# Kernel optimization log

Measured on AMD Instinct MI355X. Metric: run time of the kernel, lower is better.

The kernel has to match this reference:

```python
import jax, jax.numpy as jnp
import numpy as np

B, H, M, K = 256, 1024, 20, 20  # batch, hidden, max_ingr, pairing top_k (must be equal: M==K)
VOCAB, INGR_V = 32000, 5000


def setup_inputs() -> dict:
    key = jax.random.key(0)
    ks = jax.random.split(key, 24)
    s = 0.02
    inp = {
        "input_ids": jax.random.randint(ks[0], (1, B), 0, VOCAB),
        "hidden": jax.random.normal(ks[1], (1, B, H), jnp.float32),
        "encoder_outputs": jax.random.normal(ks[2], (M, B, 2 * H), jnp.float32),
        "input_tensor": jax.random.randint(ks[3], (B, M), 0, INGR_V),
        "pairing_ids": jax.random.randint(ks[4], (INGR_V, K), 0, INGR_V),
        # parameters
        "emb_dec": jax.random.normal(ks[5], (VOCAB, H), jnp.float32) * s,
        "enc_emb": jax.random.normal(ks[6], (INGR_V, 2 * H), jnp.float32) * s,
        "Wq_i": jax.random.normal(ks[7], (H, H), jnp.float32) * s,
        "Wk_i": jax.random.normal(ks[8], (2 * H, H), jnp.float32) * s,
        "wa_i": jax.random.normal(ks[9], (H,), jnp.float32) * s,
        "Wq_p": jax.random.normal(ks[10], (H, H), jnp.float32) * s,
        "Wk_p": jax.random.normal(ks[11], (2 * H, H), jnp.float32) * s,
        "wa_p": jax.random.normal(ks[12], (H,), jnp.float32) * s,
        "ba_p": jax.random.normal(ks[13], (), jnp.float32) * s,
        "W_lin": jax.random.normal(ks[14], (3 * H, 2 * H), jnp.float32) * s,
        "b_lin": jnp.zeros((2 * H,), jnp.float32),
        "W_ih": jax.random.normal(ks[15], (3 * H, 2 * H), jnp.float32) * s,
        "W_hh": jax.random.normal(ks[16], (3 * H, H), jnp.float32) * s,
        "b_ih": jnp.zeros((3 * H,), jnp.float32),
        "b_hh": jnp.zeros((3 * H,), jnp.float32),
        "W_out": jax.random.normal(ks[17], (H, VOCAB), jnp.float32) * s,
        "b_out": jnp.zeros((VOCAB,), jnp.float32),
    }
    return inp


def reference(input_ids, hidden, encoder_outputs, input_tensor, pairing_ids,
              emb_dec, enc_emb, Wq_i, Wk_i, wa_i, Wq_p, Wk_p, wa_p, ba_p,
              W_lin, b_lin, W_ih, W_hh, b_ih, b_hh, W_out, b_out):
    h = hidden[0]                              # (B, H)
    emb = jnp.take(emb_dec, input_ids[0], axis=0)  # (B, H)

    # ---- IngrAtt (additive attention over ingredients) ----
    # torch code does a raw .view(B, M, 2H) on a (M, B, 2H) tensor -> plain reshape
    enc = encoder_outputs.reshape(B, M, 2 * H)
    query = h @ Wq_i                           # (B, H)
    key = enc @ Wk_i                           # (B, M, H)
    scores_i = jnp.tanh(query[:, None, :] + key) @ wa_i  # (B, M)
    aw = jax.nn.softmax(scores_i, axis=-1)     # (B, M)

    # ---- retrieval: pick most-attended ingredient, gather its top-k pairings ----
    ingr_arg = jnp.argmax(aw, axis=1)                          # (B,)
    ingr_id = input_tensor[jnp.arange(B), ingr_arg]            # (B,)
    comp_ids = jnp.take(pairing_ids, ingr_id, axis=0)          # (B, K)
    comp_emb = jnp.take(enc_emb, comp_ids, axis=0)             # (B, K, 2H)

    # ---- PairingAtt ----
    q_p = h @ Wq_p                             # (B, H)
    k_p = comp_emb @ Wk_p                      # (B, K, H)
    s_p = jnp.tanh(q_p[:, None, :] + k_p) @ wa_p + ba_p  # (B, K)
    a_p = jax.nn.softmax(s_p, axis=-1)
    attn_scores = a_p * s_p                    # (B, K) softmax-weighted raw scores
    attn_app = jnp.einsum('bk,bkd->bd', attn_scores, comp_emb)  # (B, 2H)

    out_pair = jnp.concatenate([emb, attn_app], axis=-1)  # (B, 3H)
    x = out_pair @ W_lin + b_lin                           # (B, 2H) -> GRU input

    # ---- single GRU step (torch gate ordering r,z,n) ----
    gi = x @ W_ih.T + b_ih
    gh = h @ W_hh.T + b_hh
    i_r, i_z, i_n = jnp.split(gi, 3, axis=-1)
    h_r, h_z, h_n = jnp.split(gh, 3, axis=-1)
    r = jax.nn.sigmoid(i_r + h_r)
    z = jax.nn.sigmoid(i_z + h_z)
    n = jnp.tanh(i_n + r * h_n)
    h_new = (1.0 - z) * n + z * h              # (B, H)

    logits = h_new @ W_out + b_out             # (B, VOCAB)
    return logits
```

## Files before the change

kernel.cpp:

```cpp
#include <hip/hip_runtime.h>
#include <cstdio>


using f32x4   = __attribute__((ext_vector_type(4))) float;
using bf16x8  = __attribute__((ext_vector_type(8))) short;
using ushort8 = __attribute__((ext_vector_type(8))) unsigned short;

__device__ __forceinline__ unsigned short f2bf(float x) {
    unsigned u = __builtin_bit_cast(unsigned, x);
    u += 0x7fffu + ((u >> 16) & 1u);
    return (unsigned short)(u >> 16);
}
__device__ __forceinline__ float bf2f(unsigned short u) {
    return __builtin_bit_cast(float, ((unsigned)u) << 16);
}

__device__ __forceinline__ void gload16(const void* g, void* l) {
    auto gp = (const __attribute__((address_space(1))) void*)g;
    auto lp = (__attribute__((address_space(3))) void*)l;
    __builtin_amdgcn_global_load_lds(gp, lp, 16, 0, 0);
}

__global__ __launch_bounds__(256) void prep_conv_kernel(
    const float* __restrict__ hidden, const float* __restrict__ enc_out,
    const float* __restrict__ enc_emb,
    unsigned short* __restrict__ hb, unsigned short* __restrict__ encb,
    unsigned short* __restrict__ encembb)
{
    int i = blockIdx.x * 256 + threadIdx.x;
    const float* src; unsigned short* dst; int j;
    if (i < 65536)            { src = hidden;  dst = hb;      j = i; }
    else if (i < 2686976)     { src = enc_out; dst = encb;    j = i - 65536; }
    else                      { src = enc_emb; dst = encembb; j = i - 2686976; }
    float4 v = ((const float4*)src)[j];
    ((ushort4*)dst)[j] = make_ushort4(f2bf(v.x), f2bf(v.y), f2bf(v.z), f2bf(v.w));
}

__global__ __launch_bounds__(256) void conv2w_kernel(
    const float* __restrict__ Wih, const float* __restrict__ Whh,
    unsigned short* __restrict__ ob0, unsigned short* __restrict__ ob1)
{
    int i = blockIdx.x * 256 + threadIdx.x;
    const float* src; unsigned short* dst; int j;
    if (i < 1572864) { src = Wih; dst = ob0; j = i; }
    else             { src = Whh; dst = ob1; j = i - 1572864; }
    float4 v = ((const float4*)src)[j];
    ((ushort4*)dst)[j] = make_ushort4(f2bf(v.x), f2bf(v.y), f2bf(v.z), f2bf(v.w));
}

__device__ __forceinline__ void transpose_body(
    const float* __restrict__ in, unsigned short* __restrict__ out, int R, int C)
{
    __shared__ float t[32][129];
    const int tid = threadIdx.x;
    const int c0 = blockIdx.x * 32, r0 = blockIdx.y * 128;
    const int lr = tid >> 3;
    const int cc = (tid & 7) * 4;
    #pragma unroll
    for (int i = 0; i < 4; ++i) {
        int r = lr + 32 * i;
        float4 v = *(const float4*)(in + (size_t)(r0 + r) * C + c0 + cc);
        t[cc + 0][r] = v.x; t[cc + 1][r] = v.y;
        t[cc + 2][r] = v.z; t[cc + 3][r] = v.w;
    }
    __syncthreads();
    const int rc = (tid & 15) * 8;
    #pragma unroll
    for (int p = 0; p < 2; ++p) {
        int c = (tid >> 4) + 16 * p;
        const float* src = &t[c][rc];
        ushort8 o;
        #pragma unroll
        for (int j = 0; j < 8; ++j) o[j] = f2bf(src[j]);
        *(ushort8*)(out + (size_t)(c0 + c) * R + r0 + rc) = o;
    }
}
__global__ __launch_bounds__(256) void transpose1_kernel(
    const float* in, unsigned short* out, int R, int C)
{ transpose_body(in, out, R, C); }

__global__ __launch_bounds__(256) void transpose2_kernel(
    const float* in0, const float* in1, unsigned short* out0, unsigned short* out1,
    int R, int C)
{ transpose_body(blockIdx.z ? in1 : in0, blockIdx.z ? out1 : out0, R, C); }

template<int OUTBF, bool HAS_BIAS>
__device__ __forceinline__ void gemm_core(
    const unsigned short* __restrict__ A, const unsigned short* __restrict__ Bt,
    const float* __restrict__ bias, void* __restrict__ Cout, int Ncols,
    int sA, int sB, int kLen,
    unsigned short* lA0, unsigned short* lA1,
    unsigned short* lB0, unsigned short* lB1)
{
    const int tid = threadIdx.x;
    const int lane = tid & 63, wave = tid >> 6;
    const int wr = wave >> 1, wc = wave & 1;
    const int m0 = blockIdx.y * 128, n0 = blockIdx.x * 128;
    const int srow = tid >> 3, schunk = tid & 7;
    const int lm = lane & 15, lk = (lane >> 4) * 8;

    f32x4 acc[4][4];
    #pragma unroll
    for (int m = 0; m < 4; ++m)
        #pragma unroll
        for (int n = 0; n < 4; ++n) { f32x4 z = {0.f,0.f,0.f,0.f}; acc[m][n] = z; }

    const unsigned short* Ag = A  + (size_t)(m0 + srow) * sA + schunk * 8;
    const unsigned short* Bg = Bt + (size_t)(n0 + srow) * sB + schunk * 8;
    const int nt = kLen >> 6;

    auto stage = [&](unsigned short* la_, unsigned short* lb_, int t) {
        char* la = (char*)la_ + tid * 16;
        char* lb = (char*)lb_ + tid * 16;
        #pragma unroll
        for (int i = 0; i < 4; ++i) {
            gload16(Ag + (size_t)(32 * i) * sA + t * 64, la + i * 4096);
            gload16(Bg + (size_t)(32 * i) * sB + t * 64, lb + i * 4096);
        }
    };
    auto compute = [&](const unsigned short* la_, const unsigned short* lb_) {
        #pragma unroll
        for (int kk = 0; kk < 2; ++kk) {
            bf16x8 af[4], bv[4];
            #pragma unroll
            for (int m = 0; m < 4; ++m)
                af[m] = *(const bf16x8*)((const char*)la_ +
                          (wr * 64 + m * 16 + lm) * 128 + (kk * 32 + lk) * 2);
            #pragma unroll
            for (int n = 0; n < 4; ++n)
                bv[n] = *(const bf16x8*)((const char*)lb_ +
                          (wc * 64 + n * 16 + lm) * 128 + (kk * 32 + lk) * 2);
            #pragma unroll
            for (int m = 0; m < 4; ++m)
                #pragma unroll
                for (int n = 0; n < 4; ++n)
                    acc[m][n] = __builtin_amdgcn_mfma_f32_16x16x32_bf16(
                        af[m], bv[n], acc[m][n], 0, 0, 0);
        }
    };

    stage(lA0, lB0, 0);
    __syncthreads();
    for (int t = 0; t < nt; t += 2) {
        if (t + 1 < nt) stage(lA1, lB1, t + 1);
        compute(lA0, lB0);
        __syncthreads();
        if (t + 1 < nt) {
            if (t + 2 < nt) stage(lA0, lB0, t + 2);
            compute(lA1, lB1);
            __syncthreads();
        }
    }

    const int rbase = m0 + wr * 64 + (lane >> 4) * 4;
    const int cbase = n0 + wc * 64 + lm;
    #pragma unroll
    for (int m = 0; m < 4; ++m) {
        #pragma unroll
        for (int n = 0; n < 4; ++n) {
            int col = cbase + n * 16;
            float bvv = HAS_BIAS ? bias[col] : 0.0f;
            #pragma unroll
            for (int j = 0; j < 4; ++j) {
                int row = rbase + m * 16 + j;
                float v = acc[m][n][j] + bvv;
                if (OUTBF)
                    ((unsigned short*)Cout)[(size_t)row * Ncols + col] = f2bf(v);
                else
                    ((float*)Cout)[(size_t)row * Ncols + col] = v;
            }
        }
    }
}

#define GEMM_SHARED \
    __shared__ unsigned short lA0[8192]; __shared__ unsigned short lA1[8192]; \
    __shared__ unsigned short lB0[8192]; __shared__ unsigned short lB1[8192];

__global__ __launch_bounds__(256) void gemm_dual_kernel(
    const unsigned short* A, const unsigned short* B0, const unsigned short* B1,
    float* P0, float* P1)
{
    GEMM_SHARED
    const int g = blockIdx.z >> 2, s = blockIdx.z & 3;
    const unsigned short* Bt = (g ? B1 : B0) + s * 256;
    float* C = (g ? P1 : P0) + (size_t)s * 262144;
    gemm_core<0,false>(A + s * 256, Bt, nullptr, C, 1024, 1024, 1024, 256,
                       lA0, lA1, lB0, lB1);
}

__global__ __launch_bounds__(256) void reduceq_kernel(
    const float* __restrict__ pqQ, const float* __restrict__ pqP,
    float* __restrict__ query, float* __restrict__ qp)
{
    int i = blockIdx.x * 256 + threadIdx.x;
    const float4* p; float4* o; int j;
    if (i < 65536) { p = (const float4*)pqQ; o = (float4*)query; j = i; }
    else           { p = (const float4*)pqP; o = (float4*)qp;    j = i - 65536; }
    float4 a = p[j], b = p[j + 65536], c = p[j + 131072], d = p[j + 196608];
    o[j] = make_float4(a.x + b.x + c.x + d.x, a.y + b.y + c.y + d.y,
                       a.z + b.z + c.z + d.z, a.w + b.w + c.w + d.w);
}

__global__ __launch_bounds__(256) void gemm24_kernel(
    const unsigned short* encembb, const unsigned short* encb,
    const unsigned short* WkpT, const unsigned short* WkiT,
    unsigned short* kp_all, unsigned short* key)
{
    GEMM_SHARED
    const int z = blockIdx.z;
    const unsigned short* A  = z ? encb : encembb;
    const unsigned short* Bt = z ? WkiT : WkpT;
    unsigned short* C = z ? key : kp_all;
    gemm_core<1,false>(A, Bt, nullptr, C, 1024, 2048, 2048, 2048,
                       lA0, lA1, lB0, lB1);
}

__global__ __launch_bounds__(256) void gemm5_kernel(
    const unsigned short* A, const unsigned short* Bt, float* P)
{
    GEMM_SHARED
    const int z = blockIdx.z;
    gemm_core<0,false>(A + z * 768, Bt + z * 768, nullptr,
                       P + (size_t)z * 524288, 2048, 3072, 3072, 768,
                       lA0, lA1, lB0, lB1);
}

__global__ __launch_bounds__(256) void gemm67_kernel(
    const unsigned short* xb, const unsigned short* hb,
    const unsigned short* Wih, const unsigned short* Whh, float* pg)
{
    GEMM_SHARED
    const int g = blockIdx.z >> 1, s = blockIdx.z & 1;
    const unsigned short* A  = g ? hb  + s * 512 : xb  + s * 1024;
    const unsigned short* Bt = g ? Whh + s * 512 : Wih + s * 1024;
    const int sAB  = g ? 1024 : 2048;
    const int kLen = g ? 512  : 1024;
    float* C = pg + (size_t)blockIdx.z * 786432;
    gemm_core<0,false>(A, Bt, nullptr, C, 3072, sAB, sAB, kLen, lA0, lA1, lB0, lB1);
}

__global__ __launch_bounds__(512) void gemm8_fused_kernel(
    const unsigned short* __restrict__ A, const float* __restrict__ Wout,
    const float* __restrict__ bias, float* __restrict__ C)
{
    __shared__ unsigned short lA0[16384]; __shared__ unsigned short lA1[16384];
    __shared__ unsigned short lB0[8192];  __shared__ unsigned short lB1[8192];
    const int tid  = threadIdx.x;
    const int lane = tid & 63, wave = tid >> 6;
    const int wr = wave >> 1, wc = wave & 1;
    const int n0 = blockIdx.x * 128;
    const int lm = lane & 15, lk = (lane >> 4) * 8;
    const int srow = tid >> 3, schunk = tid & 7;
    const int bcol = tid & 127, bko = tid >> 7;
    const int bsw  = (bcol & 7) << 4;

    f32x4 acc[4][4];
    #pragma unroll
    for (int m = 0; m < 4; ++m)
        #pragma unroll
        for (int n = 0; n < 4; ++n) { f32x4 z = {0.f,0.f,0.f,0.f}; acc[m][n] = z; }

    const unsigned short* Ag = A + (size_t)srow * 1024 + schunk * 8;

    auto stageA = [&](unsigned short* la_, int t) {
        char* la = (char*)la_ + tid * 16;
        #pragma unroll
        for (int i = 0; i < 4; ++i)
            gload16(Ag + (size_t)(64 * i) * 1024 + t * 64, la + i * 8192);
    };
    float bv_[16];
    auto loadB = [&](int t) {
        const float* src = Wout + (size_t)(t * 64 + bko * 16) * 32000 + n0 + bcol;
        #pragma unroll
        for (int j = 0; j < 16; ++j) bv_[j] = src[(size_t)j * 32000];
    };
    auto writeB = [&](unsigned short* lb_) {
        ushort8 o0, o1;
        #pragma unroll
        for (int j = 0; j < 8; ++j) { o0[j] = f2bf(bv_[j]); o1[j] = f2bf(bv_[j + 8]); }
        char* base = (char*)lb_ + bcol * 128;
        *(ushort8*)(base + ((bko * 32)      ^ bsw)) = o0;
        *(ushort8*)(base + ((bko * 32 + 16) ^ bsw)) = o1;
    };
    auto compute = [&](const unsigned short* la_, const unsigned short* lb_) {
        #pragma unroll
        for (int kk = 0; kk < 2; ++kk) {
            bf16x8 af[4], bv[4];
            #pragma unroll
            for (int m = 0; m < 4; ++m)
                af[m] = *(const bf16x8*)((const char*)la_ +
                          (wr * 64 + m * 16 + lm) * 128 + (kk * 32 + lk) * 2);
            #pragma unroll
            for (int n = 0; n < 4; ++n) {
                int r = wc * 64 + n * 16 + lm;
                bv[n] = *(const bf16x8*)((const char*)lb_ +
                          r * 128 + (((kk * 32 + lk) * 2) ^ ((r & 7) << 4)));
            }
            #pragma unroll
            for (int m = 0; m < 4; ++m)
                #pragma unroll
                for (int n = 0; n < 4; ++n)
                    acc[m][n] = __builtin_amdgcn_mfma_f32_16x16x32_bf16(
                        af[m], bv[n], acc[m][n], 0, 0, 0);
        }
    };

    stageA(lA0, 0); loadB(0); writeB(lB0);
    __syncthreads();
    const int nt = 16;
    for (int t = 0; t < nt; t += 2) {
        if (t + 1 < nt) { stageA(lA1, t + 1); loadB(t + 1); }
        compute(lA0, lB0);
        if (t + 1 < nt) writeB(lB1);
        __syncthreads();
        if (t + 1 < nt) {
            if (t + 2 < nt) { stageA(lA0, t + 2); loadB(t + 2); }
            compute(lA1, lB1);
            if (t + 2 < nt) writeB(lB0);
            __syncthreads();
        }
    }

    const int rbase = wr * 64 + (lane >> 4) * 4;
    const int cbase = n0 + wc * 64 + lm;
    #pragma unroll
    for (int m = 0; m < 4; ++m) {
        #pragma unroll
        for (int n = 0; n < 4; ++n) {
            int col = cbase + n * 16;
            float bvv = bias[col];
            #pragma unroll
            for (int j = 0; j < 4; ++j)
                C[(size_t)(rbase + m * 16 + j) * 32000 + col] = acc[m][n][j] + bvv;
        }
    }
}

__global__ __launch_bounds__(256) void attn_scores_kernel(
    const float* __restrict__ q, const unsigned short* __restrict__ k,
    const float* __restrict__ wa, float* __restrict__ scores)
{
    const int bm = blockIdx.x;
    const int b  = bm / 20;
    const int tid = threadIdx.x;
    float4 qv  = ((const float4*)(q + (size_t)b * 1024))[tid];
    ushort4 kv = ((const ushort4*)(k + (size_t)bm * 1024))[tid];
    float4 wv  = ((const float4*)wa)[tid];
    float p = tanhf(qv.x + bf2f(kv.x)) * wv.x + tanhf(qv.y + bf2f(kv.y)) * wv.y
            + tanhf(qv.z + bf2f(kv.z)) * wv.z + tanhf(qv.w + bf2f(kv.w)) * wv.w;
    #pragma unroll
    for (int off = 32; off > 0; off >>= 1) p += __shfl_down(p, off);
    __shared__ float sp[4];
    if ((tid & 63) == 0) sp[tid >> 6] = p;
    __syncthreads();
    if (tid == 0) scores[bm] = sp[0] + sp[1] + sp[2] + sp[3];
}

__device__ __forceinline__ int argmax_ing(
    const float* __restrict__ sc_i, const int* __restrict__ input_tensor, int b)
{
    float best = sc_i[b * 20]; int bi = 0;
    #pragma unroll
    for (int m = 1; m < 20; ++m) {
        float v = sc_i[b * 20 + m];
        if (v > best) { best = v; bi = m; }
    }
    return input_tensor[b * 20 + bi];
}

__global__ __launch_bounds__(256) void attn_scores_gather_kernel(
    const float* __restrict__ q, const unsigned short* __restrict__ kp_all,
    const float* __restrict__ wa, const float* __restrict__ ba,
    const float* __restrict__ sc_i, const int* __restrict__ input_tensor,
    const int* __restrict__ pairing_ids, float* __restrict__ scores)
{
    const int bm = blockIdx.x;
    const int b  = bm / 20;
    const int kk = bm - b * 20;
    const int tid = threadIdx.x;
    const int ing = argmax_ing(sc_i, input_tensor, b);
    const int cid = pairing_ids[ing * 20 + kk];
    float4 qv  = ((const float4*)(q + (size_t)b * 1024))[tid];
    ushort4 kv = ((const ushort4*)(kp_all + (size_t)cid * 1024))[tid];
    float4 wv  = ((const float4*)wa)[tid];
    float p = tanhf(qv.x + bf2f(kv.x)) * wv.x + tanhf(qv.y + bf2f(kv.y)) * wv.y
            + tanhf(qv.z + bf2f(kv.z)) * wv.z + tanhf(qv.w + bf2f(kv.w)) * wv.w;
    #pragma unroll
    for (int off = 32; off > 0; off >>= 1) p += __shfl_down(p, off);
    __shared__ float sp[4];
    if ((tid & 63) == 0) sp[tid >> 6] = p;
    __syncthreads();
    if (tid == 0) scores[bm] = sp[0] + sp[1] + sp[2] + sp[3] + ba[0];
}

__global__ __launch_bounds__(256) void out_pair_kernel(
    const float* __restrict__ s_p, const float* __restrict__ enc_emb,
    const float* __restrict__ sc_i, const int* __restrict__ input_tensor,
    const int* __restrict__ pairing_ids,
    const float* __restrict__ emb_dec, const int* __restrict__ input_ids,
    unsigned short* __restrict__ out_pairb)
{
    const int b = blockIdx.x / 6, seg = blockIdx.x % 6;
    const int tid = threadIdx.x;
    const int d = seg * 512 + tid * 2;
    ushort2 o;
    if (seg < 2) {
        float2 v = *(const float2*)(emb_dec + (size_t)input_ids[b] * 1024 + d);
        o.x = f2bf(v.x); o.y = f2bf(v.y);
    } else {
        const int ing = argmax_ing(sc_i, input_tensor, b);
        __shared__ float s_raw[20];
        if (tid < 20) s_raw[tid] = s_p[b * 20 + tid];
        __syncthreads();
        float mx = -1e30f;
        #pragma unroll
        for (int m = 0; m < 20; ++m) mx = fmaxf(mx, s_raw[m]);
        float den = 0.f; float w[20];
        #pragma unroll
        for (int m = 0; m < 20; ++m) { w[m] = expf(s_raw[m] - mx); den += w[m]; }
        const float inv = 1.f / den;
        const int dd = d - 1024;
        float a0 = 0.f, a1 = 0.f;
        #pragma unroll
        for (int k = 0; k < 20; ++k) {
            const int cid = pairing_ids[ing * 20 + k];
            float2 v = *(const float2*)(enc_emb + (size_t)cid * 2048 + dd);
            float a = w[k] * inv * s_raw[k];
            a0 += a * v.x; a1 += a * v.y;
        }
        o.x = f2bf(a0); o.y = f2bf(a1);
    }
    *(ushort2*)(out_pairb + (size_t)b * 3072 + d) = o;
}

__global__ __launch_bounds__(256) void reduce5_kernel(
    const float* __restrict__ P, const float* __restrict__ bias,
    unsigned short* __restrict__ xb)
{
    int i = blockIdx.x * 256 + threadIdx.x;
    const float4* p = (const float4*)P;
    float4 a = p[i], b = p[i + 131072], c = p[i + 262144], d = p[i + 393216];
    float4 bb = ((const float4*)bias)[i & 511];
    ((ushort4*)xb)[i] = make_ushort4(f2bf(a.x + b.x + c.x + d.x + bb.x),
                                     f2bf(a.y + b.y + c.y + d.y + bb.y),
                                     f2bf(a.z + b.z + c.z + d.z + bb.z),
                                     f2bf(a.w + b.w + c.w + d.w + bb.w));
}

__global__ __launch_bounds__(256) void gru_kernel(
    const float* __restrict__ pg, const float* __restrict__ b_ih,
    const float* __restrict__ b_hh, const float* __restrict__ h,
    unsigned short* __restrict__ hnewb)
{
    int idx = blockIdx.x * 256 + threadIdx.x;
    int b = idx >> 10, j = idx & 1023;
    const float* gi0 = pg + (size_t)b * 3072;
    const float* gi1 = gi0 + 786432;
    const float* gh0 = gi0 + 2 * 786432;
    const float* gh1 = gi0 + 3 * 786432;
    float ir  = gi0[j]        + gi1[j]        + b_ih[j];
    float iz  = gi0[1024 + j] + gi1[1024 + j] + b_ih[1024 + j];
    float in_ = gi0[2048 + j] + gi1[2048 + j] + b_ih[2048 + j];
    float hr  = gh0[j]        + gh1[j]        + b_hh[j];
    float hz  = gh0[1024 + j] + gh1[1024 + j] + b_hh[1024 + j];
    float hn  = gh0[2048 + j] + gh1[2048 + j] + b_hh[2048 + j];
    float r = 1.f / (1.f + expf(-(ir + hr)));
    float z = 1.f / (1.f + expf(-(iz + hz)));
    float n = tanhf(in_ + r * hn);
    hnewb[idx] = f2bf((1.f - z) * n + z * h[idx]);
}

extern "C" void kernel_launch(void* const* d_in, const int* in_sizes, int n_in,
                              void* d_out, int out_size, void* d_ws, size_t ws_size,
                              hipStream_t stream)
{
    const int*   input_ids    = (const int*)  d_in[0];
    const float* hidden       = (const float*)d_in[1];
    const float* enc_out      = (const float*)d_in[2];
    const int*   input_tensor = (const int*)  d_in[3];
    const int*   pairing_ids  = (const int*)  d_in[4];
    const float* emb_dec      = (const float*)d_in[5];
    const float* enc_emb      = (const float*)d_in[6];
    const float* Wq_i  = (const float*)d_in[7];
    const float* Wk_i  = (const float*)d_in[8];
    const float* wa_i  = (const float*)d_in[9];
    const float* Wq_p  = (const float*)d_in[10];
    const float* Wk_p  = (const float*)d_in[11];
    const float* wa_p  = (const float*)d_in[12];
    const float* ba_p  = (const float*)d_in[13];
    const float* W_lin = (const float*)d_in[14];
    const float* b_lin = (const float*)d_in[15];
    const float* W_ih  = (const float*)d_in[16];
    const float* W_hh  = (const float*)d_in[17];
    const float* b_ih  = (const float*)d_in[18];
    const float* b_hh  = (const float*)d_in[19];
    const float* W_out = (const float*)d_in[20];
    const float* b_out = (const float*)d_in[21];

    constexpr size_t OFF_HB    = 0;
    constexpr size_t OFF_HNEW  = 524288;
    constexpr size_t OFF_WQI   = 1048576;
    constexpr size_t OFF_WQP   = 3145728;
    constexpr size_t OFF_WKI   = 5242880;
    constexpr size_t OFF_WKP   = 9437184;
    constexpr size_t OFF_ENC   = 13631488;
    constexpr size_t OFF_SLOT1 = 34603008;
    constexpr size_t OFF_SLOT2 = 55574528;
    constexpr size_t OFF_QUERY = 76546048;
    constexpr size_t OFF_QP    = 77594624;
    constexpr size_t OFF_SCI   = 78643200;
    constexpr size_t OFF_SCP   = 78667776;
    constexpr size_t OFF_PGI   = 1048576;
    constexpr size_t NEED      = 79167488;
    if (ws_size < NEED) {
        fprintf(stderr, "kernel_launch: ws_size %zu < needed %zu\n", ws_size, NEED);
        return;
    }
    char* ws = (char*)d_ws;
    unsigned short* hb     = (unsigned short*)(ws + OFF_HB);
    unsigned short* hnewb  = (unsigned short*)(ws + OFF_HNEW);
    unsigned short* WqiT   = (unsigned short*)(ws + OFF_WQI);
    unsigned short* WqpT   = (unsigned short*)(ws + OFF_WQP);
    float*          pqQ    = (float*)         (ws + OFF_WKI);
    float*          pqP    = (float*)         (ws + OFF_WKP);
    unsigned short* WkiT   = (unsigned short*)(ws + OFF_WKI);
    unsigned short* WkpT   = (unsigned short*)(ws + OFF_WKP);
    unsigned short* encb   = (unsigned short*)(ws + OFF_ENC);
    unsigned short* kp_all = (unsigned short*)(ws + OFF_SLOT1);
    unsigned short* key    = (unsigned short*)(ws + OFF_SLOT1 + 10485760);
    unsigned short* encembb= (unsigned short*)(ws + OFF_SLOT2);
    unsigned short* WlinT  = (unsigned short*)(ws + OFF_SLOT2);
    unsigned short* Wihb   = (unsigned short*)(ws + OFF_SLOT2);
    unsigned short* Whhb   = (unsigned short*)(ws + OFF_SLOT2 + 12582912);
    unsigned short* outp   = (unsigned short*)(ws + OFF_SLOT1);
    float*          pG5    = (float*)         (ws + OFF_SLOT1 + 1572864);
    unsigned short* xb     = (unsigned short*)(ws + OFF_SLOT1 + 9961472);
    float*          query  = (float*)         (ws + OFF_QUERY);
    float*          qp     = (float*)         (ws + OFF_QP);
    float*          sc_i   = (float*)         (ws + OFF_SCI);
    float*          sc_p   = (float*)         (ws + OFF_SCP);
    float*          pgi    = (float*)         (ws + OFF_PGI);

    prep_conv_kernel<<<20496, 256, 0, stream>>>(hidden, enc_out, enc_emb,
                                                hb, encb, encembb);

    transpose2_kernel<<<dim3(32, 8, 2), 256, 0, stream>>>(Wq_i, Wq_p, WqiT, WqpT, 1024, 1024);
    gemm_dual_kernel<<<dim3(8, 2, 8), 256, 0, stream>>>(hb, WqiT, WqpT, pqQ, pqP);
    reduceq_kernel<<<512, 256, 0, stream>>>(pqQ, pqP, query, qp);

    transpose2_kernel<<<dim3(32, 16, 2), 256, 0, stream>>>(Wk_i, Wk_p, WkiT, WkpT, 2048, 1024);

    gemm24_kernel<<<dim3(8, 40, 2), 256, 0, stream>>>(encembb, encb, WkpT, WkiT,
                                                      kp_all, key);

    attn_scores_kernel<<<5120, 256, 0, stream>>>(query, key, wa_i, sc_i);
    attn_scores_gather_kernel<<<5120, 256, 0, stream>>>(qp, kp_all, wa_p, ba_p,
                                                        sc_i, input_tensor, pairing_ids, sc_p);

    out_pair_kernel<<<1536, 256, 0, stream>>>(sc_p, enc_emb, sc_i, input_tensor,
                                              pairing_ids, emb_dec, input_ids, outp);

    transpose1_kernel<<<dim3(64, 24), 256, 0, stream>>>(W_lin, WlinT, 3072, 2048);
    gemm5_kernel<<<dim3(16, 2, 4), 256, 0, stream>>>(outp, WlinT, pG5);
    reduce5_kernel<<<512, 256, 0, stream>>>(pG5, b_lin, xb);

    conv2w_kernel<<<9216, 256, 0, stream>>>(W_ih, W_hh, Wihb, Whhb);
    gemm67_kernel<<<dim3(24, 2, 4), 256, 0, stream>>>(xb, hb, Wihb, Whhb, pgi);

    gru_kernel<<<1024, 256, 0, stream>>>(pgi, b_ih, b_hh, hidden, hnewb);

    gemm8_fused_kernel<<<250, 512, 0, stream>>>(hnewb, W_out, b_out, (float*)d_out);
}
```

Measured before the change: 257.5 us.

## Fuse prep transposes, remap gemm24 blocks per XCD, deepen split-K, retile output GEMM

Merges the activation bf16 conversion and the Wq/Wk transposes into one prep launch, which saves two launches. The gemm24 grid is flattened and remapped so each XCD works on a contiguous band of M tiles, aiming for better L2 reuse. Split-K depth is doubled for gemm5 and gemm67, with the reduce and GRU kernels summing more partials, so small GEMMs fill more CUs at the cost of extra partial-sum traffic. The final vocab GEMM moves from 512-thread 128-column tiles to 256-thread 64-column tiles with 500 blocks, which raises occupancy but re-reads the hidden-state A tile more often.

```diff
diff --git a/kernel.cpp b/kernel.cpp
--- a/kernel.cpp
+++ b/kernel.cpp
@@ -21,20 +21,69 @@
     __builtin_amdgcn_global_load_lds(gp, lp, 16, 0, 0);
 }
 
-__global__ __launch_bounds__(256) void prep_conv_kernel(
+__device__ __forceinline__ void transpose_body(
+    const float* __restrict__ in, unsigned short* __restrict__ out,
+    int R, int C, int r0, int c0)
+{
+    __shared__ float t[32][129];
+    const int tid = threadIdx.x;
+    const int lr = tid >> 3;
+    const int cc = (tid & 7) * 4;
+    #pragma unroll
+    for (int i = 0; i < 4; ++i) {
+        int r = lr + 32 * i;
+        float4 v = *(const float4*)(in + (size_t)(r0 + r) * C + c0 + cc);
+        t[cc + 0][r] = v.x; t[cc + 1][r] = v.y;
+        t[cc + 2][r] = v.z; t[cc + 3][r] = v.w;
+    }
+    __syncthreads();
+    const int rc = (tid & 15) * 8;
+    #pragma unroll
+    for (int p = 0; p < 2; ++p) {
+        int c = (tid >> 4) + 16 * p;
+        const float* src = &t[c][rc];
+        ushort8 o;
+        #pragma unroll
+        for (int j = 0; j < 8; ++j) o[j] = f2bf(src[j]);
+        *(ushort8*)(out + (size_t)(c0 + c) * R + r0 + rc) = o;
+    }
+}
+
+__global__ __launch_bounds__(256) void prep1_kernel(
     const float* __restrict__ hidden, const float* __restrict__ enc_out,
     const float* __restrict__ enc_emb,
+    const float* __restrict__ Wq_i, const float* __restrict__ Wq_p,
+    const float* __restrict__ Wk_i, const float* __restrict__ Wk_p,
     unsigned short* __restrict__ hb, unsigned short* __restrict__ encb,
-    unsigned short* __restrict__ encembb)
-{
-    int i = blockIdx.x * 256 + threadIdx.x;
-    const float* src; unsigned short* dst; int j;
-    if (i < 65536)            { src = hidden;  dst = hb;      j = i; }
-    else if (i < 2686976)     { src = enc_out; dst = encb;    j = i - 65536; }
-    else                      { src = enc_emb; dst = encembb; j = i - 2686976; }
-    float4 v = ((const float4*)src)[j];
-    ((ushort4*)dst)[j] = make_ushort4(f2bf(v.x), f2bf(v.y), f2bf(v.z), f2bf(v.w));
-}
+    unsigned short* __restrict__ encembb,
+    unsigned short* __restrict__ WqiT, unsigned short* __restrict__ WqpT,
+    unsigned short* __restrict__ WkiT, unsigned short* __restrict__ WkpT)
+{
+    const int bid = blockIdx.x;
+    if (bid < 20496) {
+        int i = bid * 256 + threadIdx.x;
+        const float* src; unsigned short* dst; int j;
+        if (i < 65536)        { src = hidden;  dst = hb;      j = i; }
+        else if (i < 2686976) { src = enc_out; dst = encb;    j = i - 65536; }
+        else                  { src = enc_emb; dst = encembb; j = i - 2686976; }
+        float4 v = ((const float4*)src)[j];
+        ((ushort4*)dst)[j] = make_ushort4(f2bf(v.x), f2bf(v.y), f2bf(v.z), f2bf(v.w));
+    } else if (bid < 21008) {
+        int local = bid - 20496;
+        int bz = local >> 8, rem = local & 255;
+        transpose_body(bz ? Wq_p : Wq_i, bz ? WqpT : WqiT,
+                       1024, 1024, (rem >> 5) * 128, (rem & 31) * 32);
+    } else {
+        int local = bid - 21008;
+        int bz = local >> 9, rem = local & 511;
+        transpose_body(bz ? Wk_p : Wk_i, bz ? WkpT : WkiT,
+                       2048, 1024, (rem >> 5) * 128, (rem & 31) * 32);
+    }
+}
+
+__global__ __launch_bounds__(256) void transpose1_kernel(
+    const float* in, unsigned short* out, int R, int C)
+{ transpose_body(in, out, R, C, blockIdx.y * 128, blockIdx.x * 32); }
 
 __global__ __launch_bounds__(256) void conv2w_kernel(
     const float* __restrict__ Wih, const float* __restrict__ Whh,
@@ -48,54 +97,17 @@
     ((ushort4*)dst)[j] = make_ushort4(f2bf(v.x), f2bf(v.y), f2bf(v.z), f2bf(v.w));
 }
 
-__device__ __forceinline__ void transpose_body(
-    const float* __restrict__ in, unsigned short* __restrict__ out, int R, int C)
-{
-    __shared__ float t[32][129];
-    const int tid = threadIdx.x;
-    const int c0 = blockIdx.x * 32, r0 = blockIdx.y * 128;
-    const int lr = tid >> 3;
-    const int cc = (tid & 7) * 4;
-    #pragma unroll
-    for (int i = 0; i < 4; ++i) {
-        int r = lr + 32 * i;
-        float4 v = *(const float4*)(in + (size_t)(r0 + r) * C + c0 + cc);
-        t[cc + 0][r] = v.x; t[cc + 1][r] = v.y;
-        t[cc + 2][r] = v.z; t[cc + 3][r] = v.w;
-    }
-    __syncthreads();
-    const int rc = (tid & 15) * 8;
-    #pragma unroll
-    for (int p = 0; p < 2; ++p) {
-        int c = (tid >> 4) + 16 * p;
-        const float* src = &t[c][rc];
-        ushort8 o;
-        #pragma unroll
-        for (int j = 0; j < 8; ++j) o[j] = f2bf(src[j]);
-        *(ushort8*)(out + (size_t)(c0 + c) * R + r0 + rc) = o;
-    }
-}
-__global__ __launch_bounds__(256) void transpose1_kernel(
-    const float* in, unsigned short* out, int R, int C)
-{ transpose_body(in, out, R, C); }
-
-__global__ __launch_bounds__(256) void transpose2_kernel(
-    const float* in0, const float* in1, unsigned short* out0, unsigned short* out1,
-    int R, int C)
-{ transpose_body(blockIdx.z ? in1 : in0, blockIdx.z ? out1 : out0, R, C); }
-
 template<int OUTBF, bool HAS_BIAS>
 __device__ __forceinline__ void gemm_core(
     const unsigned short* __restrict__ A, const unsigned short* __restrict__ Bt,
     const float* __restrict__ bias, void* __restrict__ Cout, int Ncols,
-    int sA, int sB, int kLen,
+    int sA, int sB, int kLen, int m0, int n0,
     unsigned short* lA0, unsigned short* lA1,
     unsigned short* lB0, unsigned short* lB1)
 {
     const int tid = threadIdx.x;
     const int lane = tid & 63, wave = tid >> 6;
     const int wr = wave >> 1, wc = wave & 1;
-    const int m0 = blockIdx.y * 128, n0 = blockIdx.x * 128;
     const int srow = tid >> 3, schunk = tid & 7;
     const int lm = lane & 15, lk = (lane >> 4) * 8;
 
@@ -186,7 +198,7 @@
     const unsigned short* Bt = (g ? B1 : B0) + s * 256;
     float* C = (g ? P1 : P0) + (size_t)s * 262144;
     gemm_core<0,false>(A + s * 256, Bt, nullptr, C, 1024, 1024, 1024, 256,
-                       lA0, lA1, lB0, lB1);
+                       blockIdx.y * 128, blockIdx.x * 128, lA0, lA1, lB0, lB1);
 }
 
 __global__ __launch_bounds__(256) void reduceq_kernel(
@@ -208,12 +220,17 @@
     unsigned short* kp_all, unsigned short* key)
 {
     GEMM_SHARED
-    const int z = blockIdx.z;
+    const int id  = blockIdx.x;
+    const int xcd = id & 7;
+    const int z   = xcd >> 2, q = xcd & 3;
+    const int r   = id >> 3;
+    const int mi  = q * 10 + (r >> 3);
+    const int n   = r & 7;
     const unsigned short* A  = z ? encb : encembb;
     const unsigned short* Bt = z ? WkiT : WkpT;
     unsigned short* C = z ? key : kp_all;
     gemm_core<1,false>(A, Bt, nullptr, C, 1024, 2048, 2048, 2048,
-                       lA0, lA1, lB0, lB1);
+                       mi * 128, n * 128, lA0, lA1, lB0, lB1);
 }
 
 __global__ __launch_bounds__(256) void gemm5_kernel(
@@ -221,9 +238,9 @@
 {
     GEMM_SHARED
     const int z = blockIdx.z;
-    gemm_core<0,false>(A + z * 768, Bt + z * 768, nullptr,
-                       P + (size_t)z * 524288, 2048, 3072, 3072, 768,
-                       lA0, lA1, lB0, lB1);
+    gemm_core<0,false>(A + z * 384, Bt + z * 384, nullptr,
+                       P + (size_t)z * 524288, 2048, 3072, 3072, 384,
+                       blockIdx.y * 128, blockIdx.x * 128, lA0, lA1, lB0, lB1);
 }
 
 __global__ __launch_bounds__(256) void gemm67_kernel(
@@ -231,28 +248,28 @@
     const unsigned short* Wih, const unsigned short* Whh, float* pg)
 {
     GEMM_SHARED
-    const int g = blockIdx.z >> 1, s = blockIdx.z & 1;
-    const unsigned short* A  = g ? hb  + s * 512 : xb  + s * 1024;
-    const unsigned short* Bt = g ? Whh + s * 512 : Wih + s * 1024;
+    const int g = blockIdx.z >> 2, s = blockIdx.z & 3;
+    const unsigned short* A  = g ? hb  + s * 256 : xb  + s * 512;
+    const unsigned short* Bt = g ? Whh + s * 256 : Wih + s * 512;
     const int sAB  = g ? 1024 : 2048;
-    const int kLen = g ? 512  : 1024;
+    const int kLen = g ? 256  : 512;
     float* C = pg + (size_t)blockIdx.z * 786432;
-    gemm_core<0,false>(A, Bt, nullptr, C, 3072, sAB, sAB, kLen, lA0, lA1, lB0, lB1);
-}
-
-__global__ __launch_bounds__(512) void gemm8_fused_kernel(
+    gemm_core<0,false>(A, Bt, nullptr, C, 3072, sAB, sAB, kLen,
+                       blockIdx.y * 128, blockIdx.x * 128, lA0, lA1, lB0, lB1);
+}
+
+__global__ __launch_bounds__(256) void gemm8_kernel(
     const unsigned short* __restrict__ A, const float* __restrict__ Wout,
     const float* __restrict__ bias, float* __restrict__ C)
 {
     __shared__ unsigned short lA0[16384]; __shared__ unsigned short lA1[16384];
-    __shared__ unsigned short lB0[8192];  __shared__ unsigned short lB1[8192];
+    __shared__ unsigned short lB0[4096];  __shared__ unsigned short lB1[4096];
     const int tid  = threadIdx.x;
     const int lane = tid & 63, wave = tid >> 6;
-    const int wr = wave >> 1, wc = wave & 1;
-    const int n0 = blockIdx.x * 128;
+    const int n0 = blockIdx.x * 64;
     const int lm = lane & 15, lk = (lane >> 4) * 8;
     const int srow = tid >> 3, schunk = tid & 7;
-    const int bcol = tid & 127, bko = tid >> 7;
+    const int bcol = tid & 63, bkg = tid >> 6;
     const int bsw  = (bcol & 7) << 4;
 
     f32x4 acc[4][4];
@@ -266,12 +283,12 @@
     auto stageA = [&](unsigned short* la_, int t) {
         char* la = (char*)la_ + tid * 16;
         #pragma unroll
-        for (int i = 0; i < 4; ++i)
-            gload16(Ag + (size_t)(64 * i) * 1024 + t * 64, la + i * 8192);
+        for (int i = 0; i < 8; ++i)
+            gload16(Ag + (size_t)(32 * i) * 1024 + t * 64, la + i * 4096);
     };
     float bv_[16];
     auto loadB = [&](int t) {
-        const float* src = Wout + (size_t)(t * 64 + bko * 16) * 32000 + n0 + bcol;
+        const float* src = Wout + (size_t)(t * 64 + bkg * 16) * 32000 + n0 + bcol;
         #pragma unroll
         for (int j = 0; j < 16; ++j) bv_[j] = src[(size_t)j * 32000];
     };
@@ -280,8 +297,8 @@
         #pragma unroll
         for (int j = 0; j < 8; ++j) { o0[j] = f2bf(bv_[j]); o1[j] = f2bf(bv_[j + 8]); }
         char* base = (char*)lb_ + bcol * 128;
-        *(ushort8*)(base + ((bko * 32)      ^ bsw)) = o0;
-        *(ushort8*)(base + ((bko * 32 + 16) ^ bsw)) = o1;
+        *(ushort8*)(base + ((bkg * 32)      ^ bsw)) = o0;
+        *(ushort8*)(base + ((bkg * 32 + 16) ^ bsw)) = o1;
     };
     auto compute = [&](const unsigned short* la_, const unsigned short* lb_) {
         #pragma unroll
@@ -290,12 +307,12 @@
             #pragma unroll
             for (int m = 0; m < 4; ++m)
                 af[m] = *(const bf16x8*)((const char*)la_ +
-                          (wr * 64 + m * 16 + lm) * 128 + (kk * 32 + lk) * 2);
+                          (wave * 64 + m * 16 + lm) * 128 + (kk * 32 + lk) * 2);
             #pragma unroll
             for (int n = 0; n < 4; ++n) {
-                int r = wc * 64 + n * 16 + lm;
+                int rr = n * 16 + lm;
                 bv[n] = *(const bf16x8*)((const char*)lb_ +
-                          r * 128 + (((kk * 32 + lk) * 2) ^ ((r & 7) << 4)));
+                          rr * 128 + (((kk * 32 + lk) * 2) ^ ((rr & 7) << 4)));
             }
             #pragma unroll
             for (int m = 0; m < 4; ++m)
@@ -322,8 +339,8 @@
         }
     }
 
-    const int rbase = wr * 64 + (lane >> 4) * 4;
-    const int cbase = n0 + wc * 64 + lm;
+    const int rbase = wave * 64 + (lane >> 4) * 4;
+    const int cbase = n0 + lm;
     #pragma unroll
     for (int m = 0; m < 4; ++m) {
         #pragma unroll
@@ -440,12 +457,14 @@
 {
     int i = blockIdx.x * 256 + threadIdx.x;
     const float4* p = (const float4*)P;
-    float4 a = p[i], b = p[i + 131072], c = p[i + 262144], d = p[i + 393216];
     float4 bb = ((const float4*)bias)[i & 511];
-    ((ushort4*)xb)[i] = make_ushort4(f2bf(a.x + b.x + c.x + d.x + bb.x),
-                                     f2bf(a.y + b.y + c.y + d.y + bb.y),
-                                     f2bf(a.z + b.z + c.z + d.z + bb.z),
-                                     f2bf(a.w + b.w + c.w + d.w + bb.w));
+    float s0 = bb.x, s1 = bb.y, s2 = bb.z, s3 = bb.w;
+    #pragma unroll
+    for (int s = 0; s < 8; ++s) {
+        float4 v = p[i + s * 131072];
+        s0 += v.x; s1 += v.y; s2 += v.z; s3 += v.w;
+    }
+    ((ushort4*)xb)[i] = make_ushort4(f2bf(s0), f2bf(s1), f2bf(s2), f2bf(s3));
 }
 
 __global__ __launch_bounds__(256) void gru_kernel(
@@ -455,16 +474,15 @@
 {
     int idx = blockIdx.x * 256 + threadIdx.x;
     int b = idx >> 10, j = idx & 1023;
-    const float* gi0 = pg + (size_t)b * 3072;
-    const float* gi1 = gi0 + 786432;
-    const float* gh0 = gi0 + 2 * 786432;
-    const float* gh1 = gi0 + 3 * 786432;
-    float ir  = gi0[j]        + gi1[j]        + b_ih[j];
-    float iz  = gi0[1024 + j] + gi1[1024 + j] + b_ih[1024 + j];
-    float in_ = gi0[2048 + j] + gi1[2048 + j] + b_ih[2048 + j];
-    float hr  = gh0[j]        + gh1[j]        + b_hh[j];
-    float hz  = gh0[1024 + j] + gh1[1024 + j] + b_hh[1024 + j];
-    float hn  = gh0[2048 + j] + gh1[2048 + j] + b_hh[2048 + j];
+    float ir = b_ih[j], iz = b_ih[1024 + j], in_ = b_ih[2048 + j];
+    float hr = b_hh[j], hz = b_hh[1024 + j], hn  = b_hh[2048 + j];
+    #pragma unroll
+    for (int s = 0; s < 4; ++s) {
+        const float* gi = pg + (size_t)s * 786432 + (size_t)b * 3072;
+        ir  += gi[j]; iz += gi[1024 + j]; in_ += gi[2048 + j];
+        const float* gh = pg + (size_t)(4 + s) * 786432 + (size_t)b * 3072;
+        hr  += gh[j]; hz += gh[1024 + j]; hn  += gh[2048 + j];
+    }
     float r = 1.f / (1.f + expf(-(ir + hr)));
     float z = 1.f / (1.f + expf(-(iz + hz)));
     float n = tanhf(in_ + r * hn);
@@ -522,11 +540,11 @@
     unsigned short* hnewb  = (unsigned short*)(ws + OFF_HNEW);
     unsigned short* WqiT   = (unsigned short*)(ws + OFF_WQI);
     unsigned short* WqpT   = (unsigned short*)(ws + OFF_WQP);
-    float*          pqQ    = (float*)         (ws + OFF_WKI);
-    float*          pqP    = (float*)         (ws + OFF_WKP);
     unsigned short* WkiT   = (unsigned short*)(ws + OFF_WKI);
     unsigned short* WkpT   = (unsigned short*)(ws + OFF_WKP);
     unsigned short* encb   = (unsigned short*)(ws + OFF_ENC);
+    float*          pqQ    = (float*)         (ws + OFF_SLOT1);
+    float*          pqP    = (float*)         (ws + OFF_SLOT1 + 4194304);
     unsigned short* kp_all = (unsigned short*)(ws + OFF_SLOT1);
     unsigned short* key    = (unsigned short*)(ws + OFF_SLOT1 + 10485760);
     unsigned short* encembb= (unsigned short*)(ws + OFF_SLOT2);
@@ -535,24 +553,22 @@
     unsigned short* Whhb   = (unsigned short*)(ws + OFF_SLOT2 + 12582912);
     unsigned short* outp   = (unsigned short*)(ws + OFF_SLOT1);
     float*          pG5    = (float*)         (ws + OFF_SLOT1 + 1572864);
-    unsigned short* xb     = (unsigned short*)(ws + OFF_SLOT1 + 9961472);
+    unsigned short* xb     = (unsigned short*)(ws + OFF_SLOT1 + 18350080);
     float*          query  = (float*)         (ws + OFF_QUERY);
     float*          qp     = (float*)         (ws + OFF_QP);
     float*          sc_i   = (float*)         (ws + OFF_SCI);
     float*          sc_p   = (float*)         (ws + OFF_SCP);
     float*          pgi    = (float*)         (ws + OFF_PGI);
 
-    prep_conv_kernel<<<20496, 256, 0, stream>>>(hidden, enc_out, enc_emb,
-                                                hb, encb, encembb);
-
-    transpose2_kernel<<<dim3(32, 8, 2), 256, 0, stream>>>(Wq_i, Wq_p, WqiT, WqpT, 1024, 1024);
+    prep1_kernel<<<22032, 256, 0, stream>>>(hidden, enc_out, enc_emb,
+                                            Wq_i, Wq_p, Wk_i, Wk_p,
+                                            hb, encb, encembb,
+                                            WqiT, WqpT, WkiT, WkpT);
+
     gemm_dual_kernel<<<dim3(8, 2, 8), 256, 0, stream>>>(hb, WqiT, WqpT, pqQ, pqP);
     reduceq_kernel<<<512, 256, 0, stream>>>(pqQ, pqP, query, qp);
 
-    transpose2_kernel<<<dim3(32, 16, 2), 256, 0, stream>>>(Wk_i, Wk_p, WkiT, WkpT, 2048, 1024);
-
-    gemm24_kernel<<<dim3(8, 40, 2), 256, 0, stream>>>(encembb, encb, WkpT, WkiT,
-                                                      kp_all, key);
+    gemm24_kernel<<<640, 256, 0, stream>>>(encembb, encb, WkpT, WkiT, kp_all, key);
 
     attn_scores_kernel<<<5120, 256, 0, stream>>>(query, key, wa_i, sc_i);
     attn_scores_gather_kernel<<<5120, 256, 0, stream>>>(qp, kp_all, wa_p, ba_p,
@@ -562,13 +578,13 @@
                                               pairing_ids, emb_dec, input_ids, outp);
 
     transpose1_kernel<<<dim3(64, 24), 256, 0, stream>>>(W_lin, WlinT, 3072, 2048);
-    gemm5_kernel<<<dim3(16, 2, 4), 256, 0, stream>>>(outp, WlinT, pG5);
+    gemm5_kernel<<<dim3(16, 2, 8), 256, 0, stream>>>(outp, WlinT, pG5);
     reduce5_kernel<<<512, 256, 0, stream>>>(pG5, b_lin, xb);
 
     conv2w_kernel<<<9216, 256, 0, stream>>>(W_ih, W_hh, Wihb, Whhb);
-    gemm67_kernel<<<dim3(24, 2, 4), 256, 0, stream>>>(xb, hb, Wihb, Whhb, pgi);
+    gemm67_kernel<<<dim3(24, 2, 8), 256, 0, stream>>>(xb, hb, Wihb, Whhb, pgi);
 
     gru_kernel<<<1024, 256, 0, stream>>>(pgi, b_ih, b_hh, hidden, hnewb);
 
-    gemm8_fused_kernel<<<250, 512, 0, stream>>>(hnewb, W_out, b_out, (float*)d_out);
-}
+    gemm8_kernel<<<500, 256, 0, stream>>>(hnewb, W_out, b_out, (float*)d_out);
+}
```

Result: faster. 249.9 us (-3.0%).
